# Performance work log

Measured on AMD Instinct MI355X. Metric: run time of the kernel, lower is better.

Reference implementation:

```python
import jax, jax.numpy as jnp
import numpy as np

NUM_WIRES = 14
N_LAYERS = 4
BATCH = 128


def _rx_mat(theta):
    # PennyLane RX(t) = [[cos(t/2), -i sin(t/2)], [-i sin(t/2), cos(t/2)]]
    c = jnp.cos(theta / 2).astype(jnp.complex64)
    s = jnp.sin(theta / 2).astype(jnp.complex64)
    row0 = jnp.stack([c, -1j * s], axis=-1)
    row1 = jnp.stack([-1j * s, c], axis=-1)
    return jnp.stack([row0, row1], axis=-2)  # (..., 2, 2)


def _rz_mat(theta):
    # PennyLane RZ(t) = diag(exp(-it/2), exp(it/2))
    e0 = jnp.exp(-1j * theta.astype(jnp.complex64) / 2)
    e1 = jnp.exp(1j * theta.astype(jnp.complex64) / 2)
    z = jnp.zeros_like(e0)
    row0 = jnp.stack([e0, z], axis=-1)
    row1 = jnp.stack([z, e1], axis=-1)
    return jnp.stack([row0, row1], axis=-2)


def _apply_1q(psi, gate, wire):
    # psi: (B, 2, 2, ..., 2); gate: (2,2) shared or (B,2,2) per-sample
    axis = wire + 1
    psi = jnp.moveaxis(psi, axis, -1)
    if gate.ndim == 2:
        psi = psi @ gate.T
    else:
        psi = jnp.einsum('b...j,bij->b...i', psi, gate)
    return jnp.moveaxis(psi, -1, axis)


def _apply_cnot(psi, ctrl, tgt):
    ac, at = ctrl + 1, tgt + 1
    psi0 = jnp.take(psi, 0, axis=ac)
    psi1 = jnp.take(psi, 1, axis=ac)
    at_adj = at - (1 if at > ac else 0)  # target axis shifts after removing ctrl axis
    psi1 = jnp.flip(psi1, axis=at_adj)   # X on target when ctrl=1
    return jnp.stack([psi0, psi1], axis=ac)


def _circuit(x, weights):
    # x: (B, n) real angles; weights: (L, n, 2)
    B = x.shape[0]
    n = NUM_WIRES
    psi = jnp.zeros((B,) + (2,) * n, jnp.complex64)
    psi = psi.at[(slice(None),) + (0,) * n].set(1.0)  # |0...0>
    # data encoding: per-sample RX gates
    for i in range(n):
        psi = _apply_1q(psi, _rx_mat(x[:, i]), i)
    # variational ansatz
    for l in range(N_LAYERS):
        for i in range(n):
            psi = _apply_1q(psi, _rx_mat(weights[l, i, 0]), i)
            psi = _apply_1q(psi, _rz_mat(weights[l, i, 1]), i)
        for i in range(n - 1):
            psi = _apply_cnot(psi, i, i + 1)
        psi = _apply_cnot(psi, n - 1, 0)
    # <Z_i> for every wire
    p = jnp.abs(psi) ** 2  # (B, 2, ..., 2) real
    zs = []
    for i in range(n):
        other = tuple(a for a in range(1, n + 1) if a != i + 1)
        m = jnp.sum(p, axis=other)  # (B, 2)
        zs.append(m[:, 0] - m[:, 1])
    return jnp.stack(zs, axis=-1)  # (B, n)


def setup_inputs() -> dict:
    key = jax.random.key(0)
    k1, k2, k3, k4 = jax.random.split(key, 4)
    states = jax.random.normal(k1, (BATCH, 2 ** NUM_WIRES), dtype=jnp.float32)
    weights = jax.random.normal(k2, (N_LAYERS, NUM_WIRES, 2), dtype=jnp.float32)
    lim = 1.0 / np.sqrt(NUM_WIRES)
    head_w = jax.random.uniform(k3, (1, NUM_WIRES), jnp.float32, -lim, lim)
    head_b = jax.random.uniform(k4, (1,), jnp.float32, -lim, lim)
    return {"states": states, "weights": weights, "head_w": head_w, "head_b": head_b}


def reference(states, weights, head_w, head_b):
    features = jnp.abs(states)[:, :NUM_WIRES]        # (B, n)
    qfeatures = _circuit(features, weights)          # (B, n)
    out = (qfeatures @ head_w.T + head_b)[:, 0]      # (B,)
    return out
```

## Files before the change

### kernel.cpp

```cpp
#include <hip/hip_runtime.h>
#include <math.h>

#define NW 14
#define NSTATE 16384
#define HALF 8192
#define NL 4
#define BATCH 128
#define TPB 1024
#define SHB1 (84 * 1024)


#define MAGIC64 0x9E3779B97F4A7C15ull

typedef float v2f __attribute__((ext_vector_type(2)));

#define WAVE_FENCE() __builtin_amdgcn_wave_barrier()

__device__ __forceinline__ unsigned sxmap(unsigned v) {
    unsigned t = v;
    t ^= t >> 1; t ^= t >> 2; t ^= t >> 4; t ^= t >> 8;
    return (t & 0x0FFFu) | ((t & 1u) << 13);
}

__device__ __forceinline__ float2 cmul(float2 u, float2 v) {
    return make_float2(u.x * v.x - u.y * v.y, u.x * v.y + u.y * v.x);
}

__device__ __forceinline__ void st_agent(float2* p, float2 v) {
    __hip_atomic_store(reinterpret_cast<unsigned long long*>(p),
                       __builtin_bit_cast(unsigned long long, v),
                       __ATOMIC_RELAXED, __HIP_MEMORY_SCOPE_AGENT);
}
__device__ __forceinline__ float2 ld_agent(const float2* p) {
    unsigned long long u = __hip_atomic_load(
        reinterpret_cast<const unsigned long long*>(p),
        __ATOMIC_RELAXED, __HIP_MEMORY_SCOPE_AGENT);
    return __builtin_bit_cast(float2, u);
}

__device__ __forceinline__ float4 fused_coef(const float* weights,
                                             const float* states,
                                             int b, int l, int w) {
    float t1 = weights[(l * NW + w) * 2 + 0];
    float t2 = weights[(l * NW + w) * 2 + 1];
    if (l == 0) t1 += fabsf(states[(size_t)b * NSTATE + w]);
    float s, c, sz, cz;
    sincosf(0.5f * t1, &s, &c);
    sincosf(0.5f * t2, &sz, &cz);
    return make_float4(c * cz, -c * sz, -s * sz, -s * cz);
}

template<int N, int M>
__device__ __forceinline__ void gateN(float2* rr, float4 g, unsigned s3) {
    const float f = (s3 & (unsigned)M) ? -1.0f : 1.0f;
    const v2f gx = {g.x, g.x};
    const v2f gy = {f * g.y, f * g.y};
    const v2f gz = {f * g.z, f * g.z};
    const v2f gw = {g.w, g.w};
    v2f* r = (v2f*)rr;
#pragma unroll
    for (int k = 0; k < N; ++k) {
        if ((k & M) == 0) {
            const v2f z0 = r[k], z1 = r[k|M];
            const v2f z0s = {-z0.y, z0.x};
            const v2f z1s = {-z1.y, z1.x};
            r[k]   = gx*z0 + gy*z0s + gz*z1 + gw*z1s;
            r[k|M] = gx*z1 - gy*z1s - gz*z0 + gw*z0s;
        }
    }
}

template<int J0, int S3SH, int S3MSK>
__device__ __forceinline__ void pass3h(float2* psi, const float4* gc,
                                       unsigned t) {
    const float4 gA = gc[13 - (J0 + 0)];
    const float4 gB = gc[13 - (J0 + 1)];
    const float4 gC = gc[13 - (J0 + 2)];
    const unsigned s3   = (t >> S3SH) & (unsigned)S3MSK;
    const unsigned low  = t & ((1u << J0) - 1u);
    const unsigned high = (t >> J0) << (J0 + 3);
    float2 r[8];
#pragma unroll
    for (int k = 0; k < 8; ++k)
        r[k] = psi[low | (((unsigned)k ^ s3) << J0) | high];
    gateN<8,1>(r, gA, s3);
    gateN<8,2>(r, gB, s3);
    gateN<8,4>(r, gC, s3);
#pragma unroll
    for (int k = 0; k < 8; ++k)
        psi[low | (((unsigned)k ^ s3) << J0) | high] = r[k];
}

__device__ __forceinline__ void exit_scatter(const float2* psi,
                                             float2* __restrict__ dst,
                                             float4 g1, unsigned q,
                                             unsigned tid) {
#pragma unroll
    for (int m = 0; m < 4; ++m) {
        const unsigned jc = tid + (unsigned)m * TPB;
        const float2 x0 = psi[jc];
        const float2 x1 = psi[jc | 0x1000u];
        float2 A0, A1;
        A0.x =  g1.x*x0.x - g1.y*x0.y + g1.z*x1.x - g1.w*x1.y;
        A0.y =  g1.x*x0.y + g1.y*x0.x + g1.z*x1.y + g1.w*x1.x;
        A1.x = -g1.z*x0.x - g1.w*x0.y + g1.x*x1.x + g1.y*x1.y;
        A1.y = -g1.z*x0.y + g1.w*x0.x + g1.x*x1.y - g1.y*x1.x;
        const unsigned d0 = sxmap(jc) ^ (q ? 0x1FFFu : 0u);
        st_agent(dst + d0,             A0);
        st_agent(dst + (d0 ^ 0x3FFFu), A1);
    }
}

__device__ __forceinline__ void pair_sync(unsigned long long* mine,
                                          unsigned long long* theirs,
                                          unsigned tid) {
    __syncthreads();
    if (tid == 0) {
        __hip_atomic_store(mine, MAGIC64, __ATOMIC_RELAXED,
                           __HIP_MEMORY_SCOPE_AGENT);
        while (__hip_atomic_load(theirs, __ATOMIC_RELAXED,
                                 __HIP_MEMORY_SCOPE_AGENT) != MAGIC64)
            __builtin_amdgcn_s_sleep(1);
    }
    __syncthreads();
}

__global__ __launch_bounds__(TPB) void k_fused(
    const float* __restrict__ states, const float* __restrict__ weights,
    const float* __restrict__ head_w, const float* __restrict__ head_b,
    float2* __restrict__ SA, float2* __restrict__ SB,
    unsigned long long* __restrict__ slots, float* __restrict__ out)
{
    extern __shared__ float2 psi[];
    __shared__ float2 vfac[NW][2];
    __shared__ float2 T1[128];
    __shared__ float2 T2[128];
    __shared__ float4 gcA[NW];
    __shared__ float4 gcB[NW];
    __shared__ float4 gcC[NW];
    __shared__ float wsum[TPB / 64];
    const unsigned gid = blockIdx.x, q = gid >> 7, b = gid & 127u;
    const unsigned tid = threadIdx.x;

    if (tid < NW) {
        float4 g = fused_coef(weights, states, (int)b, 0, (int)tid);
        vfac[tid][0] = make_float2(g.x, g.y);
        vfac[tid][1] = make_float2(-g.z, g.w);
    } else if (tid >= 64 && tid < 64 + NW) {
        gcA[tid - 64] = fused_coef(weights, states, (int)b, 1, (int)(tid - 64));
    } else if (tid >= 128 && tid < 128 + NW) {
        gcB[tid - 128] = fused_coef(weights, states, (int)b, 2, (int)(tid - 128));
    } else if (tid >= 192 && tid < 192 + NW) {
        gcC[tid - 192] = fused_coef(weights, states, (int)b, 3, (int)(tid - 192));
    } else if (q == 0 && tid == 256) {
        __hip_atomic_store(out + b, head_b[0], __ATOMIC_RELAXED,
                           __HIP_MEMORY_SCOPE_AGENT);
    }
    __syncthreads();

    if (tid < 128) {
        float2 p = make_float2(1.0f, 0.0f);
#pragma unroll
        for (int j = 0; j < 7; ++j)
            p = cmul(p, vfac[13 - j][(tid >> j) & 1u]);
        T1[tid] = p;
    } else if (tid < 256) {
        const unsigned u = tid - 128;
        float2 p = make_float2(1.0f, 0.0f);
#pragma unroll
        for (int j = 7; j < 14; ++j)
            p = cmul(p, vfac[13 - j][(u >> (j - 7)) & 1u]);
        T2[u] = p;
    }
    __syncthreads();

#pragma unroll
    for (int m = 0; m < 8; ++m) {
        const unsigned I  = tid + (unsigned)m * TPB;
        const unsigned If = I | (q << 13);
        const unsigned lo  = (If ^ (If >> 1)) & 0x0FFFu;
        const unsigned y12 = ((If >> 12) ^ (If >> 13) ^ If) & 1u;
        const unsigned y13 = ((If >> 13) ^ If) & 1u;
        const unsigned J = lo | (y12 << 12) | (y13 << 13);
        psi[I] = cmul(T1[J & 127u], T2[J >> 7]);
    }
    __syncthreads();

    pass3h<0, 1, 7>(psi, gcA, tid);  WAVE_FENCE();
    pass3h<3, 3, 1>(psi, gcA, tid);  WAVE_FENCE();
    pass3h<6, 0, 0>(psi, gcA, tid);  __syncthreads();
    pass3h<9, 0, 0>(psi, gcA, tid);  __syncthreads();

    exit_scatter(psi, SA + (size_t)b * NSTATE, gcA[1], q, tid);

    pair_sync(slots + (b * 4u + q),       slots + (b * 4u + (q ^ 1u)), tid);

    {
        const float4 ge = gcA[0];
        const float2* src = SA + (size_t)b * NSTATE + (size_t)q * HALF;
        float2 f0[4], f1[4];
#pragma unroll
        for (int m = 0; m < 4; ++m) {
            const unsigned ic = tid + (unsigned)m * TPB;
            f0[m] = ld_agent(src + ic);
            f1[m] = ld_agent(src + (ic ^ 0x1FFFu));
        }
#pragma unroll
        for (int m = 0; m < 4; ++m) {
            const unsigned ic = tid + (unsigned)m * TPB;
            const unsigned rc = (q ^ ic) & 1u;
            const float aar = ge.x, aai = rc ? -ge.y : ge.y;
            const float bbr = rc ? -ge.z : ge.z, bbi = ge.w;
            float2 oc, op;
            oc.x = aar*f0[m].x - aai*f0[m].y + bbr*f1[m].x - bbi*f1[m].y;
            oc.y = aar*f0[m].y + aai*f0[m].x + bbr*f1[m].y + bbi*f1[m].x;
            op.x = aar*f1[m].x + aai*f1[m].y - (bbr*f0[m].x + bbi*f0[m].y);
            op.y = aar*f1[m].y - aai*f1[m].x - (bbr*f0[m].y - bbi*f0[m].x);
            psi[ic]           = oc;
            psi[ic ^ 0x1FFFu] = op;
        }
    }
    __syncthreads();

    pass3h<0, 1, 7>(psi, gcB, tid);  WAVE_FENCE();
    pass3h<3, 3, 1>(psi, gcB, tid);  WAVE_FENCE();
    pass3h<6, 0, 0>(psi, gcB, tid);  __syncthreads();
    pass3h<9, 0, 0>(psi, gcB, tid);  __syncthreads();

    exit_scatter(psi, SB + (size_t)b * NSTATE, gcB[1], q, tid);

    pair_sync(slots + (256u + b * 4u + q), slots + (256u + b * 4u + (q ^ 1u)),
              tid);

    const unsigned h = q;
    {
        const float4 ge = gcB[0];
        const float4 g0 = gcC[0];
        const float ar = h ? -g0.z : g0.x;
        const float ai = h ?  g0.w : g0.y;
        const float br = h ?  g0.x : g0.z;
        const float bi = h ? -g0.y : g0.w;
        const float2* s0 = SB + (size_t)b * NSTATE;
        const float2* s1 = s0 + HALF;
        float2 f00[4], f01[4], f10[4], f11[4];
#pragma unroll
        for (int m = 0; m < 4; ++m) {
            const unsigned ic = tid + (unsigned)m * TPB;
            const unsigned jc = ic ^ 0x1FFFu;
            f00[m] = ld_agent(s0 + ic);
            f01[m] = ld_agent(s0 + jc);
            f10[m] = ld_agent(s1 + ic);
            f11[m] = ld_agent(s1 + jc);
        }
#pragma unroll
        for (int m = 0; m < 4; ++m) {
            const unsigned ic = tid + (unsigned)m * TPB;
            const unsigned jc = ic ^ 0x1FFFu;
            const unsigned rc = ic & 1u;
            float2 oc0, op0, oc1, op1;
            {
                const float aar = ge.x, aai = rc ? -ge.y : ge.y;
                const float bbr = rc ? -ge.z : ge.z, bbi = ge.w;
                oc0.x = aar*f00[m].x - aai*f00[m].y + bbr*f01[m].x - bbi*f01[m].y;
                oc0.y = aar*f00[m].y + aai*f00[m].x + bbr*f01[m].y + bbi*f01[m].x;
                op0.x = aar*f01[m].x + aai*f01[m].y - (bbr*f00[m].x + bbi*f00[m].y);
                op0.y = aar*f01[m].y - aai*f01[m].x - (bbr*f00[m].y - bbi*f00[m].x);
            }
            {
                const unsigned rx = rc ^ 1u;
                const float aar = ge.x, aai = rx ? -ge.y : ge.y;
                const float bbr = rx ? -ge.z : ge.z, bbi = ge.w;
                oc1.x = aar*f10[m].x - aai*f10[m].y + bbr*f11[m].x - bbi*f11[m].y;
                oc1.y = aar*f10[m].y + aai*f10[m].x + bbr*f11[m].y + bbi*f11[m].x;
                op1.x = aar*f11[m].x + aai*f11[m].y - (bbr*f10[m].x + bbi*f10[m].y);
                op1.y = aar*f11[m].y - aai*f11[m].x - (bbr*f10[m].y - bbi*f10[m].x);
            }
            float2 oA, oB;
            oA.x = ar*oc0.x - ai*oc0.y + br*oc1.x - bi*oc1.y;
            oA.y = ar*oc0.y + ai*oc0.x + br*oc1.y + bi*oc1.x;
            oB.x = ar*op0.x - ai*op0.y + br*op1.x - bi*op1.y;
            oB.y = ar*op0.y + ai*op0.x + br*op1.y + bi*op1.x;
            psi[ic] = oA;
            psi[jc] = oB;
        }
    }
    __syncthreads();

    pass3h<0, 1, 7>(psi, gcC, tid);  WAVE_FENCE();
    pass3h<3, 3, 1>(psi, gcC, tid);  WAVE_FENCE();
    pass3h<6, 0, 0>(psi, gcC, tid);  __syncthreads();
    pass3h<9, 0, 0>(psi, gcC, tid);  __syncthreads();

    float hw[NW];
#pragma unroll
    for (int i = 0; i < NW; ++i) hw[i] = head_w[i];
    float H = 0.0f, H12 = 0.0f;
#pragma unroll
    for (int i = 0; i < NW; ++i) H += hw[i];
#pragma unroll
    for (int i = 2; i < NW; ++i) H12 += hw[i];

    const float4 g1 = gcC[1];
    float acc = 0.0f;
#pragma unroll
    for (int m2 = 0; m2 < 4; ++m2) {
        const unsigned base = tid | ((unsigned)m2 << 10);
        float2 r[2];
        r[0] = psi[base];
        r[1] = psi[base | 0x1000u];
        gateN<2,1>(r, g1, 0u);
        float A = 0.0f;
        unsigned sfx = 0u;
#pragma unroll
        for (int p = 11; p >= 0; --p) {
            sfx ^= (base >> p) & 1u;
            if (sfx) A += hw[13 - p];
        }
        const unsigned P = sfx;
#pragma unroll
        for (int kk = 0; kk < 2; ++kk) {
            const unsigned u   = (unsigned)kk ^ h;
            const unsigned b13 = P ^ (unsigned)kk;
            float sum = u ? (H12 - A) : A;
            if (u)   sum += hw[1];
            if (b13) sum += hw[0];
            const float cv = H - 2.0f * sum;
            acc += (r[kk].x * r[kk].x + r[kk].y * r[kk].y) * cv;
        }
    }
#pragma unroll
    for (int off = 32; off > 0; off >>= 1)
        acc += __shfl_down(acc, off, 64);
    if ((tid & 63u) == 0) wsum[tid >> 6] = acc;
    __syncthreads();
    if (tid == 0) {
        float tot = 0.0f;
#pragma unroll
        for (int i = 0; i < TPB / 64; ++i) tot += wsum[i];
        atomicAdd(out + b, tot);
    }
}

extern "C" void kernel_launch(void* const* d_in, const int* in_sizes, int n_in,
                              void* d_out, int out_size, void* d_ws, size_t ws_size,
                              hipStream_t stream) {
    const float* states  = (const float*)d_in[0];
    const float* weights = (const float*)d_in[1];
    const float* head_w  = (const float*)d_in[2];
    const float* head_b  = (const float*)d_in[3];
    float* out = (float*)d_out;

    float2* SA = (float2*)d_ws;
    float2* SB = SA + (size_t)BATCH * NSTATE;
    unsigned long long* slots =
        (unsigned long long*)(SB + (size_t)BATCH * NSTATE);

    k_fused<<<2 * BATCH, TPB, SHB1, stream>>>(states, weights, head_w, head_b,
                                              SA, SB, slots, out);
}
```

Before: 101.7 us.

## Keep locally-consumed half of exit scatter in LDS spare buffer

```diff
diff --git a/kernel.cpp b/kernel.cpp
--- a/kernel.cpp
+++ b/kernel.cpp
@@ -7,7 +7,7 @@
 #define NL 4
 #define BATCH 128
 #define TPB 1024
-#define SHB1 (84 * 1024)
+#define SHB ((HALF + HALF / 2) * (int)sizeof(float2))
 
 
 #define MAGIC64 0x9E3779B97F4A7C15ull
@@ -91,10 +91,11 @@
         psi[low | (((unsigned)k ^ s3) << J0) | high] = r[k];
 }
 
-__device__ __forceinline__ void exit_scatter(const float2* psi,
-                                             float2* __restrict__ dst,
-                                             float4 g1, unsigned q,
-                                             unsigned tid) {
+template<bool DUAL>
+__device__ __forceinline__ void exit_split(const float2* psi, float2* spare,
+                                           float2* __restrict__ dstBase,
+                                           float4 g1, unsigned q,
+                                           unsigned tid) {
 #pragma unroll
     for (int m = 0; m < 4; ++m) {
         const unsigned jc = tid + (unsigned)m * TPB;
@@ -105,9 +106,16 @@
         A0.y =  g1.x*x0.y + g1.y*x0.x + g1.z*x1.y + g1.w*x1.x;
         A1.x = -g1.z*x0.x - g1.w*x0.y + g1.x*x1.x + g1.y*x1.y;
         A1.y = -g1.z*x0.y + g1.w*x0.x + g1.x*x1.y - g1.y*x1.x;
-        const unsigned d0 = sxmap(jc) ^ (q ? 0x1FFFu : 0u);
-        st_agent(dst + d0,             A0);
-        st_agent(dst + (d0 ^ 0x3FFFu), A1);
+        const unsigned dA = sxmap(jc) ^ (q ? 0x1FFFu : 0u);
+        const unsigned dB = dA ^ 0x3FFFu;
+        const bool Arem = ((dA >> 13) != q);
+        const unsigned ld = Arem ? dB : dA;
+        const unsigned rd = Arem ? dA : dB;
+        const float2  lv = Arem ? A1 : A0;
+        const float2  rv = Arem ? A0 : A1;
+        spare[(ld & 0x1FFFu) >> 1] = lv;
+        st_agent(dstBase + rd, rv);
+        if (DUAL) st_agent(dstBase + ld, lv);
     }
 }
 
@@ -132,6 +140,7 @@
     unsigned long long* __restrict__ slots, float* __restrict__ out)
 {
     extern __shared__ float2 psi[];
+    float2* const spare = psi + HALF;
     __shared__ float2 vfac[NW][2];
     __shared__ float2 T1[128];
     __shared__ float2 T2[128];
@@ -191,31 +200,42 @@
     pass3h<6, 0, 0>(psi, gcA, tid);  __syncthreads();
     pass3h<9, 0, 0>(psi, gcA, tid);  __syncthreads();
 
-    exit_scatter(psi, SA + (size_t)b * NSTATE, gcA[1], q, tid);
+    exit_split<false>(psi, spare, SA + (size_t)b * NSTATE, gcA[1], q, tid);
 
     pair_sync(slots + (b * 4u + q),       slots + (b * 4u + (q ^ 1u)), tid);
 
     {
         const float4 ge = gcA[0];
         const float2* src = SA + (size_t)b * NSTATE + (size_t)q * HALF;
-        float2 f0[4], f1[4];
+        float2 fo[4], fe[4];
+        unsigned icv[4];
 #pragma unroll
         for (int m = 0; m < 4; ++m) {
             const unsigned ic = tid + (unsigned)m * TPB;
-            f0[m] = ld_agent(src + ic);
-            f1[m] = ld_agent(src + (ic ^ 0x1FFFu));
-        }
-#pragma unroll
-        for (int m = 0; m < 4; ++m) {
-            const unsigned ic = tid + (unsigned)m * TPB;
+            icv[m] = ic;
+            const unsigned od = (ic & 1u) ? ic : (ic ^ 0x1FFFu);
+            fo[m] = ld_agent(src + od);
+        }
+#pragma unroll
+        for (int m = 0; m < 4; ++m) {
+            const unsigned ic = icv[m];
+            const unsigned ev = (ic & 1u) ? (ic ^ 0x1FFFu) : ic;
+            fe[m] = spare[ev >> 1];
+        }
+#pragma unroll
+        for (int m = 0; m < 4; ++m) {
+            const unsigned ic = icv[m];
+            const bool odd = (ic & 1u);
+            const float2 f0 = odd ? fo[m] : fe[m];
+            const float2 f1 = odd ? fe[m] : fo[m];
             const unsigned rc = (q ^ ic) & 1u;
             const float aar = ge.x, aai = rc ? -ge.y : ge.y;
             const float bbr = rc ? -ge.z : ge.z, bbi = ge.w;
             float2 oc, op;
-            oc.x = aar*f0[m].x - aai*f0[m].y + bbr*f1[m].x - bbi*f1[m].y;
-            oc.y = aar*f0[m].y + aai*f0[m].x + bbr*f1[m].y + bbi*f1[m].x;
-            op.x = aar*f1[m].x + aai*f1[m].y - (bbr*f0[m].x + bbi*f0[m].y);
-            op.y = aar*f1[m].y - aai*f1[m].x - (bbr*f0[m].y - bbi*f0[m].x);
+            oc.x = aar*f0.x - aai*f0.y + bbr*f1.x - bbi*f1.y;
+            oc.y = aar*f0.y + aai*f0.x + bbr*f1.y + bbi*f1.x;
+            op.x = aar*f1.x + aai*f1.y - (bbr*f0.x + bbi*f0.y);
+            op.y = aar*f1.y - aai*f1.x - (bbr*f0.y - bbi*f0.x);
             psi[ic]           = oc;
             psi[ic ^ 0x1FFFu] = op;
         }
@@ -227,7 +247,7 @@
     pass3h<6, 0, 0>(psi, gcB, tid);  __syncthreads();
     pass3h<9, 0, 0>(psi, gcB, tid);  __syncthreads();
 
-    exit_scatter(psi, SB + (size_t)b * NSTATE, gcB[1], q, tid);
+    exit_split<true>(psi, spare, SB + (size_t)b * NSTATE, gcB[1], q, tid);
 
     pair_sync(slots + (256u + b * 4u + q), slots + (256u + b * 4u + (q ^ 1u)),
               tid);
@@ -240,40 +260,55 @@
         const float ai = h ?  g0.w : g0.y;
         const float br = h ?  g0.x : g0.z;
         const float bi = h ? -g0.y : g0.w;
-        const float2* s0 = SB + (size_t)b * NSTATE;
-        const float2* s1 = s0 + HALF;
-        float2 f00[4], f01[4], f10[4], f11[4];
+        const float2* sQ = SB + (size_t)b * NSTATE + (size_t)q * HALF;
+        const float2* sP = SB + (size_t)b * NSTATE + (size_t)(q ^ 1u) * HALF;
+        float2 qo[4], pi[4], pj[4], qe[4];
+        unsigned icv[4];
 #pragma unroll
         for (int m = 0; m < 4; ++m) {
             const unsigned ic = tid + (unsigned)m * TPB;
             const unsigned jc = ic ^ 0x1FFFu;
-            f00[m] = ld_agent(s0 + ic);
-            f01[m] = ld_agent(s0 + jc);
-            f10[m] = ld_agent(s1 + ic);
-            f11[m] = ld_agent(s1 + jc);
-        }
-#pragma unroll
-        for (int m = 0; m < 4; ++m) {
-            const unsigned ic = tid + (unsigned)m * TPB;
+            icv[m] = ic;
+            const unsigned od = (ic & 1u) ? ic : jc;
+            qo[m] = ld_agent(sQ + od);
+            pi[m] = ld_agent(sP + ic);
+            pj[m] = ld_agent(sP + jc);
+        }
+#pragma unroll
+        for (int m = 0; m < 4; ++m) {
+            const unsigned ic = icv[m];
+            const unsigned ev = (ic & 1u) ? (ic ^ 0x1FFFu) : ic;
+            qe[m] = spare[ev >> 1];
+        }
+#pragma unroll
+        for (int m = 0; m < 4; ++m) {
+            const unsigned ic = icv[m];
             const unsigned jc = ic ^ 0x1FFFu;
+            const bool odd = (ic & 1u);
+            const float2 o_i = odd ? qo[m] : qe[m];
+            const float2 o_j = odd ? qe[m] : qo[m];
+            const float2 f00 = q ? pi[m] : o_i;
+            const float2 f01 = q ? pj[m] : o_j;
+            const float2 f10 = q ? o_i   : pi[m];
+            const float2 f11 = q ? o_j   : pj[m];
             const unsigned rc = ic & 1u;
             float2 oc0, op0, oc1, op1;
             {
                 const float aar = ge.x, aai = rc ? -ge.y : ge.y;
                 const float bbr = rc ? -ge.z : ge.z, bbi = ge.w;
-                oc0.x = aar*f00[m].x - aai*f00[m].y + bbr*f01[m].x - bbi*f01[m].y;
-                oc0.y = aar*f00[m].y + aai*f00[m].x + bbr*f01[m].y + bbi*f01[m].x;
-                op0.x = aar*f01[m].x + aai*f01[m].y - (bbr*f00[m].x + bbi*f00[m].y);
-                op0.y = aar*f01[m].y - aai*f01[m].x - (bbr*f00[m].y - bbi*f00[m].x);
+                oc0.x = aar*f00.x - aai*f00.y + bbr*f01.x - bbi*f01.y;
+                oc0.y = aar*f00.y + aai*f00.x + bbr*f01.y + bbi*f01.x;
+                op0.x = aar*f01.x + aai*f01.y - (bbr*f00.x + bbi*f00.y);
+                op0.y = aar*f01.y - aai*f01.x - (bbr*f00.y - bbi*f00.x);
             }
             {
                 const unsigned rx = rc ^ 1u;
                 const float aar = ge.x, aai = rx ? -ge.y : ge.y;
                 const float bbr = rx ? -ge.z : ge.z, bbi = ge.w;
-                oc1.x = aar*f10[m].x - aai*f10[m].y + bbr*f11[m].x - bbi*f11[m].y;
-                oc1.y = aar*f10[m].y + aai*f10[m].x + bbr*f11[m].y + bbi*f11[m].x;
-                op1.x = aar*f11[m].x + aai*f11[m].y - (bbr*f10[m].x + bbi*f10[m].y);
-                op1.y = aar*f11[m].y - aai*f11[m].x - (bbr*f10[m].y - bbi*f10[m].x);
+                oc1.x = aar*f10.x - aai*f10.y + bbr*f11.x - bbi*f11.y;
+                oc1.y = aar*f10.y + aai*f10.x + bbr*f11.y + bbi*f11.x;
+                op1.x = aar*f11.x + aai*f11.y - (bbr*f10.x + bbi*f10.y);
+                op1.y = aar*f11.y - aai*f11.x - (bbr*f10.y - bbi*f10.x);
             }
             float2 oA, oB;
             oA.x = ar*oc0.x - ai*oc0.y + br*oc1.x - bi*oc1.y;
@@ -355,6 +390,6 @@
     unsigned long long* slots =
         (unsigned long long*)(SB + (size_t)BATCH * NSTATE);
 
-    k_fused<<<2 * BATCH, TPB, SHB1, stream>>>(states, weights, head_w, head_b,
-                                              SA, SB, slots, out);
-}
+    k_fused<<<2 * BATCH, TPB, SHB, stream>>>(states, weights, head_w, head_b,
+                                             SA, SB, slots, out);
+}
```

Measured after the change: 98.11 us. 1.04x faster.
